# Optimization experiments

Hardware: AMD Instinct MI355X
Metric: run time of the kernel (lower is better)

Reference implementation:

```python
import jax, jax.numpy as jnp
import numpy as np

B, T, D_K, N_HEADS, D_FF, VOCAB, N_LAYERS = 4, 1024, 1024, 16, 4096, 65, 6


def setup_inputs() -> dict:
    key = jax.random.key(0)
    ks = jax.random.split(key, 12)
    f = lambda k, sh: jax.random.normal(k, sh, dtype=jnp.float32) * 0.02
    return {
        "batchData": jax.random.randint(ks[0], (B, T), 0, VOCAB),
        "target": jax.random.randint(ks[1], (B, T), 0, VOCAB),
        "pos": jnp.arange(T),
        "Wtok": f(ks[2], (VOCAB, D_K)),
        "Wpos": f(ks[3], (T, D_K)),
        "Wq": f(ks[4], (D_K, D_K)), "bq": jnp.zeros((D_K,), jnp.float32),
        "Wk": f(ks[5], (D_K, D_K)), "bk": jnp.zeros((D_K,), jnp.float32),
        "Wv": f(ks[6], (D_K, D_K)), "bv": jnp.zeros((D_K,), jnp.float32),
        "W1": f(ks[7], (D_K, D_FF)), "b1": jnp.zeros((D_FF,), jnp.float32),
        "W2": f(ks[8], (D_FF, D_K)), "b2": jnp.zeros((D_K,), jnp.float32),
        "ln_w": jnp.ones((D_K,), jnp.float32),
        "Wf": f(ks[9], (D_K, VOCAB)), "bf": jnp.zeros((VOCAB,), jnp.float32),
        "n_layers": N_LAYERS,
        "n_heads": N_HEADS,
    }


def layer_norm(x, w, eps=1e-5):
    m = jnp.mean(x, axis=-1, keepdims=True)
    v = jnp.var(x, axis=-1, keepdims=True)
    return (x - m) / jnp.sqrt(v + eps) * w


def reference(batchData, target, pos, Wtok, Wpos, Wq, bq, Wk, bk, Wv, bv,
              W1, b1, W2, b2, ln_w, Wf, bf, n_layers, n_heads):
    x = Wtok[batchData] + Wpos[pos]  # [B, T, C] (pos embedding broadcasts)
    Bsz, Tlen, C = x.shape
    dh = C // n_heads
    mask = jnp.tril(jnp.ones((Tlen, Tlen), dtype=bool))
    inv_sqrt_dk = 1.0 / jnp.sqrt(jnp.float32(C))  # source divides by sqrt(full d_k)

    def block(x):
        q = (x @ Wq + bq).reshape(Bsz, Tlen, n_heads, dh).transpose(0, 2, 1, 3)
        k = (x @ Wk + bk).reshape(Bsz, Tlen, n_heads, dh).transpose(0, 2, 1, 3)
        v = (x @ Wv + bv).reshape(Bsz, Tlen, n_heads, dh).transpose(0, 2, 1, 3)
        scores = jnp.einsum('bhqd,bhkd->bhqk', q, k) * inv_sqrt_dk
        scores = jnp.where(mask, scores, -jnp.inf)
        attn = jax.nn.softmax(scores, axis=-1)
        h = jnp.einsum('bhqk,bhkd->bhqd', attn, v)
        h = h.transpose(0, 2, 1, 3).reshape(Bsz, Tlen, C)
        h = h + layer_norm(h, ln_w)           # x = x + ln(x) (shared ln)
        ff = jax.nn.relu(h @ W1 + b1) @ W2 + b2
        return ff + layer_norm(ff, ln_w)      # same shared ln again

    # ModuleList repeats the SAME block object, so weights are shared across layers
    for _ in range(n_layers):
        x = block(x)

    logits = x @ Wf + bf                       # [B, T, V]
    probs = jax.nn.softmax(logits, axis=1)     # softmax over T, as in source
    pred = probs.reshape(Bsz * Tlen, -1)
    onehot = jax.nn.one_hot(target.reshape(-1), VOCAB, dtype=jnp.float32)
    # F.cross_entropy with soft (one-hot float) targets
    loss = -jnp.mean(jnp.sum(onehot * jax.nn.log_softmax(pred, axis=-1), axis=-1))
    return loss, probs
```

## Files before the change

kernel.cpp:

```cpp
#include <hip/hip_runtime.h>

typedef __attribute__((ext_vector_type(8))) short bh8;
typedef __attribute__((ext_vector_type(4))) float f4v;

constexpr int VOC = 65;
constexpr int NL  = 6;
constexpr int Mrow = 4096;

__device__ inline float b2f(unsigned short u) {
  union { unsigned int i; float f; } x; x.i = ((unsigned int)u) << 16; return x.f;
}
__device__ inline unsigned short f2b(float f) {
  union { float f; unsigned int i; } x; x.f = f;
  return (unsigned short)((x.i + 0x7FFFu + ((x.i >> 16) & 1u)) >> 16);
}
__device__ inline void gld16(const void* g, void* l) {
  __builtin_amdgcn_global_load_lds(
      (const __attribute__((address_space(1))) unsigned int*)g,
      (__attribute__((address_space(3))) unsigned int*)l, 16, 0, 0);
}
__device__ inline bh8 lds_swz(const unsigned short* base, int row, int colbyte) {
  int off = row * 128 + (colbyte ^ ((row & 7) << 4));
  return *(const bh8*)((const char*)base + off);
}
__device__ inline f4v mfma16(bh8 a, bh8 b, f4v c) {
  return __builtin_amdgcn_mfma_f32_16x16x32_bf16(a, b, c, 0, 0, 0);
}
#define WAITV(n) asm volatile("s_waitcnt vmcnt(" #n ")" ::: "memory")
#define WAITVL(n) asm volatile("s_waitcnt vmcnt(" #n ") lgkmcnt(0)" ::: "memory")

__global__ __launch_bounds__(256) void wt_conv(const float* __restrict__ src,
    unsigned short* __restrict__ dst, int K, int N) {
  __shared__ float t[32][33];
  int k0 = blockIdx.x * 32, n0 = blockIdx.y * 32;
  int tid = threadIdx.x;
#pragma unroll
  for (int i = 0; i < 4; ++i) {
    int idx = tid + i * 256;
    int kr = idx >> 5, nc = idx & 31;
    t[kr][nc] = (n0 + nc < N) ? src[(size_t)(k0 + kr) * N + n0 + nc] : 0.f;
  }
  __syncthreads();
#pragma unroll
  for (int i = 0; i < 4; ++i) {
    int idx = tid + i * 256;
    int nr = idx >> 5, kc = idx & 31;
    dst[(size_t)(n0 + nr) * K + k0 + kc] = f2b(t[kc][nr]);
  }
}

__global__ __launch_bounds__(256) void bias_prep(
    const float* __restrict__ bq, const float* __restrict__ bk,
    const float* __restrict__ bv, const float* __restrict__ bf,
    float* __restrict__ bqkv, float* __restrict__ bfp) {
  int i = blockIdx.x * 256 + threadIdx.x;
  if (i < 1024) bqkv[i] = bq[i];
  else if (i < 2048) bqkv[i] = bk[i - 1024];
  else if (i < 3072) bqkv[i] = bv[i - 2048];
  else if (i < 3200) bfp[i - 3072] = (i - 3072 < VOC) ? bf[i - 3072] : 0.f;
}

__global__ __launch_bounds__(256) void embed_bf(const int* __restrict__ tok,
    const float* __restrict__ Wtok, const float* __restrict__ Wpos,
    unsigned short* __restrict__ Xb) {
  int bt = blockIdx.x, t = bt & 1023, tid = threadIdx.x;
  int id = tok[bt];
  float4 a = ((const float4*)(Wtok + (size_t)id * 1024))[tid];
  float4 p = ((const float4*)(Wpos + (size_t)t * 1024))[tid];
  ushort4 o;
  o.x = f2b(a.x + p.x); o.y = f2b(a.y + p.y);
  o.z = f2b(a.z + p.z); o.w = f2b(a.w + p.w);
  ((ushort4*)(Xb + (size_t)bt * 1024))[tid] = o;
}

template <bool RELU, bool PART, bool VT>
__global__ __launch_bounds__(512) void gemm8(
    const unsigned short* __restrict__ A, const unsigned short* __restrict__ Bt,
    const float* __restrict__ bias, void* __restrict__ Cout,
    unsigned short* __restrict__ Vtout, long N, long Kloop, long lda, long ldb,
    int MT, int NT) {
  __shared__ unsigned short As[3 * 256 * 32];
  __shared__ unsigned short Bs[3 * 128 * 32];
  const int tid = threadIdx.x;
  const int lane = tid & 63, w = tid >> 6;
  const int wr = w >> 1, wc = w & 1;
  const int lr = lane & 15, lh = lane >> 4, lh4 = lh * 4;

  const int nwg = (int)gridDim.x;
  const int wid = ((int)blockIdx.x & 7) * (nwg >> 3) + ((int)blockIdx.x >> 3);
  const int rowT = wid % MT, rest = wid / MT;
  const int colT = rest % NT, ksl = rest / NT;
  const long row0 = (long)rowT * 256, col0 = (long)colT * 128;
  const long kOff = (long)ksl * Kloop;

  f4v acc[4][4];
#pragma unroll
  for (int i = 0; i < 4; ++i)
#pragma unroll
    for (int j = 0; j < 4; ++j) acc[i][j] = f4v{0.f, 0.f, 0.f, 0.f};

  const int rg = tid >> 2, s = tid & 3;
  const int ch = s ^ ((rg ^ (rg >> 2)) & 3);
  const unsigned short* ApA0 = A + (row0 + rg) * lda + kOff + ch * 8;
  const unsigned short* ApA1 = ApA0 + 128 * lda;
  const unsigned short* BpB  = Bt + (col0 + rg) * ldb + kOff + ch * 8;

  auto stage = [&](int t, int buf) {
    const long k0 = (long)t << 5;
    gld16(ApA0 + k0, &As[buf * 8192 + tid * 8]);
    gld16(ApA1 + k0, &As[buf * 8192 + 4096 + tid * 8]);
    gld16(BpB  + k0, &Bs[buf * 4096 + tid * 8]);
  };

  const int nt = (int)(Kloop >> 5);
  stage(0, 0);
  stage(1, 1);

  const int fl = (lr ^ (lr >> 2)) & 3;
  const int slot = lh ^ fl;

  for (int t = 0; t < nt; ++t) {
    if (t + 1 < nt) { WAITVL(3); } else { WAITVL(0); }
    __builtin_amdgcn_s_barrier();
    __builtin_amdgcn_sched_barrier(0);
    const unsigned short* Ab = &As[(t % 3) * 8192];
    const unsigned short* Bb = &Bs[(t % 3) * 4096];
    bh8 a[4], b[4];
#pragma unroll
    for (int mi = 0; mi < 4; ++mi)
      a[mi] = *(const bh8*)&Ab[(wr * 64 + mi * 16 + lr) * 32 + slot * 8];
#pragma unroll
    for (int ni = 0; ni < 4; ++ni)
      b[ni] = *(const bh8*)&Bb[(wc * 64 + ni * 16 + lr) * 32 + slot * 8];
    if (t + 2 < nt) stage(t + 2, (t + 2) % 3);
    __builtin_amdgcn_s_setprio(1);
#pragma unroll
    for (int mi = 0; mi < 4; ++mi)
#pragma unroll
      for (int ni = 0; ni < 4; ++ni)
        acc[mi][ni] = mfma16(a[mi], b[ni], acc[mi][ni]);
    __builtin_amdgcn_s_setprio(0);
  }

  if (PART) {
    unsigned short* P = (unsigned short*)Cout + (size_t)ksl * 4096 * 1024;
#pragma unroll
    for (int mi = 0; mi < 4; ++mi)
#pragma unroll
      for (int ni = 0; ni < 4; ++ni) {
        long col = col0 + wc * 64 + ni * 16 + lr;
#pragma unroll
        for (int r = 0; r < 4; ++r) {
          long row = row0 + wr * 64 + mi * 16 + lh4 + r;
          P[row * N + col] = f2b(acc[mi][ni][r]);
        }
      }
    return;
  }
  if (VT && col0 >= 2048) {
#pragma unroll
    for (int mi = 0; mi < 4; ++mi) {
#pragma unroll
      for (int ni = 0; ni < 4; ++ni) {
        int col = (int)col0 + wc * 64 + ni * 16 + lr;
        float bb = bias[col];
        int cc = col - 2048;
        long row = row0 + wr * 64 + mi * 16 + lh4;
        int bi = (int)(row >> 10), tt = (int)(row & 1023);
        ushort4 o;
        o.x = f2b(acc[mi][ni][0] + bb);
        o.y = f2b(acc[mi][ni][1] + bb);
        o.z = f2b(acc[mi][ni][2] + bb);
        o.w = f2b(acc[mi][ni][3] + bb);
        *(ushort4*)&Vtout[((size_t)(bi * 16 + (cc >> 6)) * 64 + (cc & 63)) *
                              1024 + tt] = o;
      }
    }
    return;
  }
#pragma unroll
  for (int mi = 0; mi < 4; ++mi) {
#pragma unroll
    for (int ni = 0; ni < 4; ++ni) {
      long col = col0 + wc * 64 + ni * 16 + lr;
      float bb = bias[col];
#pragma unroll
      for (int r = 0; r < 4; ++r) {
        long row = row0 + wr * 64 + mi * 16 + lh4 + r;
        float v = acc[mi][ni][r] + bb;
        if (RELU) v = fmaxf(v, 0.f);
        ((unsigned short*)Cout)[row * N + col] = f2b(v);
      }
    }
  }
}

template <int TM, int TN, bool RELU, bool F32OUT>
__global__ __launch_bounds__(256) void gemm4(
    const unsigned short* __restrict__ A, const unsigned short* __restrict__ Bt,
    const float* __restrict__ bias, void* __restrict__ Cout, long N, long K) {
  constexpr int MI = TM / 32, NI = TN / 32;
  constexpr int ABUF = TM * 64, BBUF = TN * 64;
  __shared__ unsigned short As[2 * ABUF];
  __shared__ unsigned short Bs[2 * BBUF];
  const int tid = threadIdx.x;
  const int lane = tid & 63, w = tid >> 6;
  const int wr = w >> 1, wc = w & 1;
  const int lr = lane & 15, lh = lane >> 4, lh4 = lh * 4;
  const long row0 = (long)blockIdx.x * TM, col0 = (long)blockIdx.y * TN;
  f4v acc[MI][NI];
#pragma unroll
  for (int i = 0; i < MI; ++i)
#pragma unroll
    for (int j = 0; j < NI; ++j) acc[i][j] = f4v{0.f, 0.f, 0.f, 0.f};
  const int rg = tid >> 3, s = tid & 7;
  const int ch = s ^ (rg & 7);
  const unsigned short* Ap = A + (row0 + rg) * K + ch * 8;
  const unsigned short* Bp = Bt + (col0 + rg) * K + ch * 8;
  auto stage = [&](int t, int buf) {
    const long k0 = (long)t << 6;
#pragma unroll
    for (int i = 0; i < MI; ++i)
      gld16(Ap + i * 32 * K + k0, &As[buf * ABUF + (i * 256 + tid) * 8]);
#pragma unroll
    for (int i = 0; i < NI; ++i)
      gld16(Bp + i * 32 * K + k0, &Bs[buf * BBUF + (i * 256 + tid) * 8]);
  };
  const int nt = (int)(K >> 6);
  stage(0, 0);
  for (int t = 0; t < nt; ++t) {
    const int cur = t & 1;
    if (t + 1 < nt) {
      stage(t + 1, cur ^ 1);
      WAITV(6);
    } else {
      WAITV(0);
    }
    __builtin_amdgcn_s_barrier();
    const unsigned short* Ab = &As[cur * ABUF];
    const unsigned short* Bb = &Bs[cur * BBUF];
#pragma unroll
    for (int ks = 0; ks < 2; ++ks) {
      bh8 a[MI], b[NI];
      const int slot = ((ks << 2) | lh) ^ (lr & 7);
#pragma unroll
      for (int mi = 0; mi < MI; ++mi) {
        int m = wr * (TM / 2) + mi * 16 + lr;
        a[mi] = *(const bh8*)((const char*)Ab + m * 128 + slot * 16);
      }
#pragma unroll
      for (int ni = 0; ni < NI; ++ni) {
        int n = wc * (TN / 2) + ni * 16 + lr;
        b[ni] = *(const bh8*)((const char*)Bb + n * 128 + slot * 16);
      }
#pragma unroll
      for (int mi = 0; mi < MI; ++mi)
#pragma unroll
        for (int ni = 0; ni < NI; ++ni)
          acc[mi][ni] = mfma16(a[mi], b[ni], acc[mi][ni]);
    }
    __builtin_amdgcn_s_barrier();
  }
#pragma unroll
  for (int mi = 0; mi < MI; ++mi) {
#pragma unroll
    for (int ni = 0; ni < NI; ++ni) {
      long col = col0 + wc * (TN / 2) + ni * 16 + lr;
      float bb = bias[col];
#pragma unroll
      for (int r = 0; r < 4; ++r) {
        long row = row0 + wr * (TM / 2) + mi * 16 + lh4 + r;
        float v = acc[mi][ni][r] + bb;
        if (RELU) v = fmaxf(v, 0.f);
        if (F32OUT) ((float*)Cout)[row * N + col] = v;
        else ((unsigned short*)Cout)[row * N + col] = f2b(v);
      }
    }
  }
}

__global__ __launch_bounds__(256) void attn_mfma(
    const unsigned short* __restrict__ QKV, const unsigned short* __restrict__ Vt,
    unsigned short* __restrict__ Hout) {
  __shared__ unsigned short Ks[2][64 * 64];
  __shared__ unsigned short Vs[2][64 * 64];
  __shared__ unsigned short Ps[4][16 * 64];
  const int tid = threadIdx.x, w = tid >> 6, lane = tid & 63;
  const int qt = (int)gridDim.x - 1 - (int)blockIdx.x;
  const int bh = blockIdx.y;
  const int b = bh >> 4, h = bh & 15;
  const int lr = lane & 15, lh = lane >> 4, lh4 = lh * 4;

  const unsigned short* qp =
      QKV + (size_t)(b * 1024 + qt * 64 + w * 16 + lr) * 3072 + h * 64 + lh * 8;
  bh8 aq0 = *(const bh8*)qp;
  bh8 aq1 = *(const bh8*)(qp + 32);

  f4v o[4];
#pragma unroll
  for (int i = 0; i < 4; ++i) o[i] = f4v{0.f, 0.f, 0.f, 0.f};
  float m = -1e30f, l = 0.f;

  const int r8 = tid >> 3, slot = tid & 7;
  unsigned short* pw = &Ps[w][0];

  auto stage = [&](int kt, int buf) {
    int r = r8, c8 = (slot ^ (r & 7)) * 8;
    gld16(QKV + (size_t)(b * 1024 + kt * 64 + r) * 3072 + 1024 + h * 64 + c8,
          &Ks[buf][tid * 8]);
    gld16(Vt + (size_t)(bh * 64 + r) * 1024 + kt * 64 + c8, &Vs[buf][tid * 8]);
    r = r8 + 32; c8 = (slot ^ (r & 7)) * 8;
    gld16(QKV + (size_t)(b * 1024 + kt * 64 + r) * 3072 + 1024 + h * 64 + c8,
          &Ks[buf][2048 + tid * 8]);
    gld16(Vt + (size_t)(bh * 64 + r) * 1024 + kt * 64 + c8,
          &Vs[buf][2048 + tid * 8]);
  };

  stage(0, 0);

  for (int kt = 0; kt <= qt; ++kt) {
    const int cur = kt & 1;
    if (kt < qt) {
      stage(kt + 1, cur ^ 1);
      WAITV(4);
    } else {
      WAITV(0);
    }
    __builtin_amdgcn_s_barrier();

    f4v s[4];
#pragma unroll
    for (int nt = 0; nt < 4; ++nt) {
      bh8 k0 = lds_swz(Ks[cur], nt * 16 + lr, lh * 16);
      bh8 k1 = lds_swz(Ks[cur], nt * 16 + lr, lh * 16 + 64);
      f4v z = f4v{0.f, 0.f, 0.f, 0.f};
      z = mfma16(k0, aq0, z);
      z = mfma16(k1, aq1, z);
      s[nt] = z;
    }
    const bool diag = (kt == qt);
    const int qloc = w * 16 + lr;
#pragma unroll
    for (int nt = 0; nt < 4; ++nt)
#pragma unroll
      for (int r = 0; r < 4; ++r) {
        float v = s[nt][r] * 0.03125f;
        if (diag && (nt * 16 + lh4 + r) > qloc) v = -1e30f;
        s[nt][r] = v;
      }
    float tm = s[0][0];
#pragma unroll
    for (int nt = 0; nt < 4; ++nt)
#pragma unroll
      for (int r = 0; r < 4; ++r) tm = fmaxf(tm, s[nt][r]);
    tm = fmaxf(tm, __shfl_xor(tm, 16));
    tm = fmaxf(tm, __shfl_xor(tm, 32));
    float mn = fmaxf(m, tm);
    float corr = __expf(m - mn);
    m = mn;
    float sum = 0.f;
#pragma unroll
    for (int nt = 0; nt < 4; ++nt)
#pragma unroll
      for (int r = 0; r < 4; ++r) {
        float e = __expf(s[nt][r] - mn);
        s[nt][r] = e;
        sum += e;
      }
    sum += __shfl_xor(sum, 16);
    sum += __shfl_xor(sum, 32);
    l = l * corr + sum;
#pragma unroll
    for (int nt = 0; nt < 4; ++nt) {
      unsigned int u0, u1;
      asm("v_cvt_pk_bf16_f32 %0, %1, %2" : "=v"(u0) : "v"(s[nt][0]), "v"(s[nt][1]));
      asm("v_cvt_pk_bf16_f32 %0, %1, %2" : "=v"(u1) : "v"(s[nt][2]), "v"(s[nt][3]));
      uint2 pk{u0, u1};
      *(uint2*)((char*)pw + lr * 128 + ((nt * 32 + lh * 8) ^ ((lr & 7) << 4))) = pk;
    }
    float c0 = __shfl(corr, lh4 + 0), c1 = __shfl(corr, lh4 + 1);
    float c2 = __shfl(corr, lh4 + 2), c3 = __shfl(corr, lh4 + 3);
#pragma unroll
    for (int nt = 0; nt < 4; ++nt) {
      o[nt][0] *= c0; o[nt][1] *= c1; o[nt][2] *= c2; o[nt][3] *= c3;
    }
    bh8 pa0 = lds_swz(pw, lr, lh * 16);
    bh8 pa1 = lds_swz(pw, lr, lh * 16 + 64);
#pragma unroll
    for (int nt = 0; nt < 4; ++nt) {
      bh8 v0 = lds_swz(Vs[cur], nt * 16 + lr, lh * 16);
      bh8 v1 = lds_swz(Vs[cur], nt * 16 + lr, lh * 16 + 64);
      o[nt] = mfma16(pa0, v0, o[nt]);
      o[nt] = mfma16(pa1, v1, o[nt]);
    }
    __builtin_amdgcn_s_barrier();
  }
  float linv = 1.f / l;
  float l0 = __shfl(linv, lh4 + 0), l1 = __shfl(linv, lh4 + 1);
  float l2 = __shfl(linv, lh4 + 2), l3 = __shfl(linv, lh4 + 3);
  const size_t rowb = (size_t)(b * 1024 + qt * 64 + w * 16);
#pragma unroll
  for (int nt = 0; nt < 4; ++nt) {
    int col = h * 64 + nt * 16 + lr;
    Hout[(rowb + lh4 + 0) * 1024 + col] = f2b(o[nt][0] * l0);
    Hout[(rowb + lh4 + 1) * 1024 + col] = f2b(o[nt][1] * l1);
    Hout[(rowb + lh4 + 2) * 1024 + col] = f2b(o[nt][2] * l2);
    Hout[(rowb + lh4 + 3) * 1024 + col] = f2b(o[nt][3] * l3);
  }
}

__global__ __launch_bounds__(256) void ln_res_bf(
    const unsigned short* __restrict__ Xi, const float* __restrict__ wln,
    unsigned short* __restrict__ Y) {
  int row = blockIdx.x, tid = threadIdx.x;
  ushort4 u = ((const ushort4*)(Xi + (size_t)row * 1024))[tid];
  float x0 = b2f(u.x), x1 = b2f(u.y), x2 = b2f(u.z), x3 = b2f(u.w);
  float s = x0 + x1 + x2 + x3;
  float ss = x0 * x0 + x1 * x1 + x2 * x2 + x3 * x3;
#pragma unroll
  for (int off = 32; off; off >>= 1) {
    s += __shfl_xor(s, off);
    ss += __shfl_xor(ss, off);
  }
  __shared__ float sw[4], ssw[4];
  int wv = tid >> 6, ln = tid & 63;
  if (ln == 0) { sw[wv] = s; ssw[wv] = ss; }
  __syncthreads();
  s = sw[0] + sw[1] + sw[2] + sw[3];
  ss = ssw[0] + ssw[1] + ssw[2] + ssw[3];
  float mean = s * (1.f / 1024.f);
  float var = ss * (1.f / 1024.f) - mean * mean;
  float rstd = rsqrtf(var + 1e-5f);
  float4 wv4 = ((const float4*)wln)[tid];
  ushort4 out;
  out.x = f2b(x0 + (x0 - mean) * rstd * wv4.x);
  out.y = f2b(x1 + (x1 - mean) * rstd * wv4.y);
  out.z = f2b(x2 + (x2 - mean) * rstd * wv4.z);
  out.w = f2b(x3 + (x3 - mean) * rstd * wv4.w);
  ((ushort4*)(Y + (size_t)row * 1024))[tid] = out;
}

__global__ __launch_bounds__(256) void ln2_fuse(
    const unsigned short* __restrict__ P, const float* __restrict__ b2,
    const float* __restrict__ wln, unsigned short* __restrict__ Y) {
  int row = blockIdx.x, tid = threadIdx.x;
  const size_t plane = (size_t)4096 * 1024;
  float x0 = 0.f, x1 = 0.f, x2 = 0.f, x3 = 0.f;
#pragma unroll
  for (int pl = 0; pl < 4; ++pl) {
    ushort4 u = *(const ushort4*)&P[pl * plane + (size_t)row * 1024 + tid * 4];
    x0 += b2f(u.x); x1 += b2f(u.y); x2 += b2f(u.z); x3 += b2f(u.w);
  }
  float4 bb = ((const float4*)b2)[tid];
  x0 += bb.x; x1 += bb.y; x2 += bb.z; x3 += bb.w;
  float s = x0 + x1 + x2 + x3;
  float ss = x0 * x0 + x1 * x1 + x2 * x2 + x3 * x3;
#pragma unroll
  for (int off = 32; off; off >>= 1) {
    s += __shfl_xor(s, off);
    ss += __shfl_xor(ss, off);
  }
  __shared__ float sw[4], ssw[4];
  int wv = tid >> 6, ln = tid & 63;
  if (ln == 0) { sw[wv] = s; ssw[wv] = ss; }
  __syncthreads();
  s = sw[0] + sw[1] + sw[2] + sw[3];
  ss = ssw[0] + ssw[1] + ssw[2] + ssw[3];
  float mean = s * (1.f / 1024.f);
  float var = ss * (1.f / 1024.f) - mean * mean;
  float rstd = rsqrtf(var + 1e-5f);
  float4 wv4 = ((const float4*)wln)[tid];
  ushort4 out;
  out.x = f2b(x0 + (x0 - mean) * rstd * wv4.x);
  out.y = f2b(x1 + (x1 - mean) * rstd * wv4.y);
  out.z = f2b(x2 + (x2 - mean) * rstd * wv4.z);
  out.w = f2b(x3 + (x3 - mean) * rstd * wv4.w);
  ((ushort4*)(Y + (size_t)row * 1024))[tid] = out;
}

__global__ __launch_bounds__(256) void softmaxT_kernel(
    const float* __restrict__ logits, float* __restrict__ probs) {
  int b = blockIdx.x / VOC;
  int v = blockIdx.x - b * VOC;
  const float* src = logits + (size_t)b * 1024 * 128 + v;
  float vals[4];
  float m = -1e30f;
#pragma unroll
  for (int i = 0; i < 4; ++i) {
    int t = threadIdx.x + 256 * i;
    vals[i] = src[(size_t)t * 128];
    m = fmaxf(m, vals[i]);
  }
#pragma unroll
  for (int off = 32; off; off >>= 1) m = fmaxf(m, __shfl_xor(m, off));
  __shared__ float sm[4], ssum[4];
  int wv = threadIdx.x >> 6, ln = threadIdx.x & 63;
  if (ln == 0) sm[wv] = m;
  __syncthreads();
  m = fmaxf(fmaxf(sm[0], sm[1]), fmaxf(sm[2], sm[3]));
  float s = 0.f;
#pragma unroll
  for (int i = 0; i < 4; ++i) { vals[i] = __expf(vals[i] - m); s += vals[i]; }
#pragma unroll
  for (int off = 32; off; off >>= 1) s += __shfl_xor(s, off);
  if (ln == 0) ssum[wv] = s;
  __syncthreads();
  s = ssum[0] + ssum[1] + ssum[2] + ssum[3];
  float inv = 1.f / s;
  float* dst = probs + (size_t)b * 1024 * VOC + v;
#pragma unroll
  for (int i = 0; i < 4; ++i) {
    int t = threadIdx.x + 256 * i;
    dst[(size_t)t * VOC] = vals[i] * inv;
  }
}

__global__ __launch_bounds__(256) void loss_rows_kernel(
    const float* __restrict__ probs, const int* __restrict__ tgt,
    float* __restrict__ partial) {
  int wv = threadIdx.x >> 6, lane = threadIdx.x & 63;
  int row = blockIdx.x * 4 + wv;
  const float* p = probs + (size_t)row * VOC;
  float x0 = p[lane];
  float x1 = (lane == 0) ? p[64] : -1e30f;
  float m = fmaxf(x0, x1);
#pragma unroll
  for (int off = 32; off; off >>= 1) m = fmaxf(m, __shfl_xor(m, off));
  float s = __expf(x0 - m) + ((lane == 0) ? __expf(x1 - m) : 0.f);
#pragma unroll
  for (int off = 32; off; off >>= 1) s += __shfl_xor(s, off);
  if (lane == 0) {
    int tg = tgt[row];
    partial[row] = (p[tg] - m) - logf(s);
  }
}

__global__ __launch_bounds__(256) void loss_final_kernel(
    const float* __restrict__ partial, float* __restrict__ out) {
  float s = 0.f;
  for (int i = threadIdx.x; i < Mrow; i += 256) s += partial[i];
#pragma unroll
  for (int off = 32; off; off >>= 1) s += __shfl_xor(s, off);
  __shared__ float sw[4];
  int wv = threadIdx.x >> 6, ln = threadIdx.x & 63;
  if (ln == 0) sw[wv] = s;
  __syncthreads();
  if (threadIdx.x == 0) out[0] = -(sw[0] + sw[1] + sw[2] + sw[3]) / (float)Mrow;
}

extern "C" void kernel_launch(void* const* d_in, const int* in_sizes, int n_in,
                              void* d_out, int out_size, void* d_ws,
                              size_t ws_size, hipStream_t stream) {
  (void)in_sizes; (void)n_in; (void)out_size; (void)ws_size;
  const int*   tok    = (const int*)d_in[0];
  const int*   target = (const int*)d_in[1];
  const float* Wtok   = (const float*)d_in[3];
  const float* Wpos   = (const float*)d_in[4];
  const float* Wq = (const float*)d_in[5];  const float* bq = (const float*)d_in[6];
  const float* Wk = (const float*)d_in[7];  const float* bk = (const float*)d_in[8];
  const float* Wv = (const float*)d_in[9];  const float* bv = (const float*)d_in[10];
  const float* W1 = (const float*)d_in[11]; const float* b1 = (const float*)d_in[12];
  const float* W2 = (const float*)d_in[13]; const float* b2 = (const float*)d_in[14];
  const float* lnw = (const float*)d_in[15];
  const float* Wf = (const float*)d_in[16]; const float* bf = (const float*)d_in[17];
  float* out = (float*)d_out;

  char* p = (char*)d_ws;
  unsigned short* Xb    = (unsigned short*)p; p += (size_t)Mrow * 1024 * 2;
  unsigned short* QKVb  = (unsigned short*)p; p += (size_t)Mrow * 3072 * 2;
  unsigned short* Vt    = (unsigned short*)p; p += (size_t)64 * 64 * 1024 * 2;
  unsigned short* Hb    = (unsigned short*)p; p += (size_t)Mrow * 1024 * 2;
  unsigned short* F2b   = (unsigned short*)p; p += (size_t)Mrow * 1024 * 2;
  unsigned short* FF1b  = (unsigned short*)p; p += (size_t)Mrow * 4096 * 2;
  unsigned short* WqkvT = (unsigned short*)p; p += (size_t)3072 * 1024 * 2;
  unsigned short* W1T   = (unsigned short*)p; p += (size_t)4096 * 1024 * 2;
  unsigned short* W2T   = (unsigned short*)p; p += (size_t)1024 * 4096 * 2;
  unsigned short* WfT   = (unsigned short*)p; p += (size_t)128 * 1024 * 2;
  float* bqkv = (float*)p; p += 3072 * 4;
  float* bfp  = (float*)p; p += 128 * 4;
  float* LOG  = (float*)p; p += (size_t)Mrow * 128 * 4;
  float* PART = (float*)p; p += Mrow * 4;
  unsigned short* Pff2 = QKVb;

  wt_conv<<<dim3(32, 32), 256, 0, stream>>>(Wq, WqkvT,                1024, 1024);
  wt_conv<<<dim3(32, 32), 256, 0, stream>>>(Wk, WqkvT + 1024 * 1024,  1024, 1024);
  wt_conv<<<dim3(32, 32), 256, 0, stream>>>(Wv, WqkvT + 2048 * 1024,  1024, 1024);
  wt_conv<<<dim3(32, 128), 256, 0, stream>>>(W1, W1T, 1024, 4096);
  wt_conv<<<dim3(128, 32), 256, 0, stream>>>(W2, W2T, 4096, 1024);
  wt_conv<<<dim3(32, 4), 256, 0, stream>>>(Wf, WfT, 1024, VOC);
  bias_prep<<<13, 256, 0, stream>>>(bq, bk, bv, bf, bqkv, bfp);

  embed_bf<<<Mrow, 256, 0, stream>>>(tok, Wtok, Wpos, Xb);

  for (int l = 0; l < NL; ++l) {
    gemm8<false, false, true><<<384, 512, 0, stream>>>(
        Xb, WqkvT, bqkv, QKVb, Vt, 3072, 1024, 1024, 1024, 16, 24);
    attn_mfma<<<dim3(16, 64), 256, 0, stream>>>(QKVb, Vt, Hb);
    ln_res_bf<<<Mrow, 256, 0, stream>>>(Hb, lnw, F2b);
    gemm8<true, false, false><<<512, 512, 0, stream>>>(
        F2b, W1T, b1, FF1b, nullptr, 4096, 1024, 1024, 1024, 16, 32);
    gemm8<false, true, false><<<512, 512, 0, stream>>>(
        FF1b, W2T, nullptr, Pff2, nullptr, 1024, 1024, 4096, 4096, 16, 8);
    ln2_fuse<<<Mrow, 256, 0, stream>>>(Pff2, b2, lnw, Xb);
  }

  gemm4<64, 128, false, true><<<dim3(64, 1), 256, 0, stream>>>(
      Xb, WfT, bfp, LOG, 128, 1024);
  softmaxT_kernel<<<4 * VOC, 256, 0, stream>>>(LOG, out + 1);
  loss_rows_kernel<<<Mrow / 4, 256, 0, stream>>>(out + 1, target, PART);
  loss_final_kernel<<<1, 256, 0, stream>>>(PART, out);
}
```

Before: 1.048 ms.

## Load attention K/V fragments directly from global, lazy softmax rescale, fold Q scale

The attention kernel drops its double-buffered LDS staging of K and V tiles and barriers. Each wave now loads its MFMA fragments straight from global memory into registers. The online softmax skips rescaling unless the running max grows by more than a threshold, which avoids the exp and multiply on the output in most iterations. The 1/sqrt(d) scale is folded into the Q projection epilogue. In exchange, each wave loads the same K/V redundantly from global/L2 with no prefetch overlap, so memory latency is exposed.

```diff
diff --git a/kernel.cpp b/kernel.cpp
--- a/kernel.cpp
+++ b/kernel.cpp
@@ -178,6 +178,7 @@
     }
     return;
   }
+  const float qsc = (VT && col0 < 1024) ? 0.03125f : 1.0f;
 #pragma unroll
   for (int mi = 0; mi < 4; ++mi) {
 #pragma unroll
@@ -188,6 +189,7 @@
       for (int r = 0; r < 4; ++r) {
         long row = row0 + wr * 64 + mi * 16 + lh4 + r;
         float v = acc[mi][ni][r] + bb;
+        if (VT) v *= qsc;
         if (RELU) v = fmaxf(v, 0.f);
         ((unsigned short*)Cout)[row * N + col] = f2b(v);
       }
@@ -282,8 +284,6 @@
 __global__ __launch_bounds__(256) void attn_mfma(
     const unsigned short* __restrict__ QKV, const unsigned short* __restrict__ Vt,
     unsigned short* __restrict__ Hout) {
-  __shared__ unsigned short Ks[2][64 * 64];
-  __shared__ unsigned short Vs[2][64 * 64];
   __shared__ unsigned short Ps[4][16 * 64];
   const int tid = threadIdx.x, w = tid >> 6, lane = tid & 63;
   const int qt = (int)gridDim.x - 1 - (int)blockIdx.x;
@@ -301,75 +301,74 @@
   for (int i = 0; i < 4; ++i) o[i] = f4v{0.f, 0.f, 0.f, 0.f};
   float m = -1e30f, l = 0.f;
 
-  const int r8 = tid >> 3, slot = tid & 7;
   unsigned short* pw = &Ps[w][0];
-
-  auto stage = [&](int kt, int buf) {
-    int r = r8, c8 = (slot ^ (r & 7)) * 8;
-    gld16(QKV + (size_t)(b * 1024 + kt * 64 + r) * 3072 + 1024 + h * 64 + c8,
-          &Ks[buf][tid * 8]);
-    gld16(Vt + (size_t)(bh * 64 + r) * 1024 + kt * 64 + c8, &Vs[buf][tid * 8]);
-    r = r8 + 32; c8 = (slot ^ (r & 7)) * 8;
-    gld16(QKV + (size_t)(b * 1024 + kt * 64 + r) * 3072 + 1024 + h * 64 + c8,
-          &Ks[buf][2048 + tid * 8]);
-    gld16(Vt + (size_t)(bh * 64 + r) * 1024 + kt * 64 + c8,
-          &Vs[buf][2048 + tid * 8]);
-  };
-
-  stage(0, 0);
+  const unsigned short* Kb =
+      QKV + (size_t)(b * 1024) * 3072 + 1024 + h * 64 + lh * 8;
+  const unsigned short* Vb = Vt + (size_t)(bh * 64) * 1024 + lh * 8;
 
   for (int kt = 0; kt <= qt; ++kt) {
-    const int cur = kt & 1;
-    if (kt < qt) {
-      stage(kt + 1, cur ^ 1);
-      WAITV(4);
-    } else {
-      WAITV(0);
-    }
-    __builtin_amdgcn_s_barrier();
+    bh8 kf0[4], kf1[4], vf0[4], vf1[4];
+#pragma unroll
+    for (int nt = 0; nt < 4; ++nt) {
+      const unsigned short* kp = Kb + (size_t)(kt * 64 + nt * 16 + lr) * 3072;
+      kf0[nt] = *(const bh8*)kp;
+      kf1[nt] = *(const bh8*)(kp + 32);
+      const unsigned short* vp = Vb + (size_t)(nt * 16 + lr) * 1024 + kt * 64;
+      vf0[nt] = *(const bh8*)vp;
+      vf1[nt] = *(const bh8*)(vp + 32);
+    }
 
     f4v s[4];
 #pragma unroll
     for (int nt = 0; nt < 4; ++nt) {
-      bh8 k0 = lds_swz(Ks[cur], nt * 16 + lr, lh * 16);
-      bh8 k1 = lds_swz(Ks[cur], nt * 16 + lr, lh * 16 + 64);
       f4v z = f4v{0.f, 0.f, 0.f, 0.f};
-      z = mfma16(k0, aq0, z);
-      z = mfma16(k1, aq1, z);
+      z = mfma16(kf0[nt], aq0, z);
+      z = mfma16(kf1[nt], aq1, z);
       s[nt] = z;
     }
     const bool diag = (kt == qt);
-    const int qloc = w * 16 + lr;
-#pragma unroll
-    for (int nt = 0; nt < 4; ++nt)
-#pragma unroll
-      for (int r = 0; r < 4; ++r) {
-        float v = s[nt][r] * 0.03125f;
-        if (diag && (nt * 16 + lh4 + r) > qloc) v = -1e30f;
-        s[nt][r] = v;
-      }
-    float tm = s[0][0];
-#pragma unroll
-    for (int nt = 0; nt < 4; ++nt)
-#pragma unroll
-      for (int r = 0; r < 4; ++r) tm = fmaxf(tm, s[nt][r]);
+    if (diag) {
+      const int qloc = w * 16 + lr;
+#pragma unroll
+      for (int nt = 0; nt < 4; ++nt)
+#pragma unroll
+        for (int r = 0; r < 4; ++r)
+          if ((nt * 16 + lh4 + r) > qloc) s[nt][r] = -1e30f;
+    }
+    float tm = fmaxf(fmaxf(fmaxf(s[0][0], s[0][1]), fmaxf(s[0][2], s[0][3])),
+                     fmaxf(fmaxf(s[1][0], s[1][1]), fmaxf(s[1][2], s[1][3])));
+    float tm2 = fmaxf(fmaxf(fmaxf(s[2][0], s[2][1]), fmaxf(s[2][2], s[2][3])),
+                      fmaxf(fmaxf(s[3][0], s[3][1]), fmaxf(s[3][2], s[3][3])));
+    tm = fmaxf(tm, tm2);
     tm = fmaxf(tm, __shfl_xor(tm, 16));
     tm = fmaxf(tm, __shfl_xor(tm, 32));
-    float mn = fmaxf(m, tm);
-    float corr = __expf(m - mn);
-    m = mn;
+
+    const bool resc = __any(tm > m + 8.f);
+    const float mu = resc ? fmaxf(m, tm) : m;
     float sum = 0.f;
 #pragma unroll
     for (int nt = 0; nt < 4; ++nt)
 #pragma unroll
       for (int r = 0; r < 4; ++r) {
-        float e = __expf(s[nt][r] - mn);
+        float e = __expf(s[nt][r] - mu);
         s[nt][r] = e;
         sum += e;
       }
     sum += __shfl_xor(sum, 16);
     sum += __shfl_xor(sum, 32);
-    l = l * corr + sum;
+    if (resc) {
+      float corr = __expf(m - mu);
+      m = mu;
+      l = l * corr + sum;
+      float c0 = __shfl(corr, lh4 + 0), c1 = __shfl(corr, lh4 + 1);
+      float c2 = __shfl(corr, lh4 + 2), c3 = __shfl(corr, lh4 + 3);
+#pragma unroll
+      for (int nt = 0; nt < 4; ++nt) {
+        o[nt][0] *= c0; o[nt][1] *= c1; o[nt][2] *= c2; o[nt][3] *= c3;
+      }
+    } else {
+      l += sum;
+    }
 #pragma unroll
     for (int nt = 0; nt < 4; ++nt) {
       unsigned int u0, u1;
@@ -378,22 +377,13 @@
       uint2 pk{u0, u1};
       *(uint2*)((char*)pw + lr * 128 + ((nt * 32 + lh * 8) ^ ((lr & 7) << 4))) = pk;
     }
-    float c0 = __shfl(corr, lh4 + 0), c1 = __shfl(corr, lh4 + 1);
-    float c2 = __shfl(corr, lh4 + 2), c3 = __shfl(corr, lh4 + 3);
-#pragma unroll
-    for (int nt = 0; nt < 4; ++nt) {
-      o[nt][0] *= c0; o[nt][1] *= c1; o[nt][2] *= c2; o[nt][3] *= c3;
-    }
     bh8 pa0 = lds_swz(pw, lr, lh * 16);
     bh8 pa1 = lds_swz(pw, lr, lh * 16 + 64);
 #pragma unroll
     for (int nt = 0; nt < 4; ++nt) {
-      bh8 v0 = lds_swz(Vs[cur], nt * 16 + lr, lh * 16);
-      bh8 v1 = lds_swz(Vs[cur], nt * 16 + lr, lh * 16 + 64);
-      o[nt] = mfma16(pa0, v0, o[nt]);
-      o[nt] = mfma16(pa1, v1, o[nt]);
-    }
-    __builtin_amdgcn_s_barrier();
+      o[nt] = mfma16(pa0, vf0[nt], o[nt]);
+      o[nt] = mfma16(pa1, vf1[nt], o[nt]);
+    }
   }
   float linv = 1.f / l;
   float l0 = __shfl(linv, lh4 + 0), l1 = __shfl(linv, lh4 + 1);
```

Result: slower. 1.487 ms (+41.9%).
